# Kernel tuning notes

Hardware: AMD Instinct MI355X
Metric: run time of the kernel (lower is better)

Reference implementation:

```python
import jax, jax.numpy as jnp
import numpy as np
from functools import partial

B, T, P, W = 32, 4096, 512, 128
NMEL, FILT, PDIM, K = 80, 256, 64, 9
PAD = (K - 1) // 2  # original uses (kernel[0][0]-1)//2 for both convs
EPS = 1e-5


def setup_inputs() -> dict:
    key = jax.random.key(0)
    ks = jax.random.split(key, 8)
    inp = {}
    inp["mask"] = jnp.zeros((B, P), dtype=bool)
    inp["mels"] = jax.random.normal(ks[0], (B, T, NMEL), dtype=jnp.float32)
    inp["mel_mask"] = jnp.zeros((B, T), dtype=bool)
    # uniform segments: 8 frames per phone (sum == T), 4 phones per word (sum == P)
    inp["durations"] = jnp.full((B, P), T // P, dtype=jnp.int32)
    inp["word_phone_len"] = jnp.full((B, W), P // W, dtype=jnp.int32)
    s1 = 1.0 / np.sqrt(NMEL * K)
    s2 = 1.0 / np.sqrt(FILT * K)
    s3 = 1.0 / np.sqrt(FILT)
    inp["conv1_w"] = jax.random.normal(ks[1], (FILT, NMEL, K), dtype=jnp.float32) * s1
    inp["conv1_b"] = jnp.zeros((FILT,), dtype=jnp.float32)
    inp["ln1_g"] = jnp.ones((FILT,), dtype=jnp.float32)
    inp["ln1_b"] = jnp.zeros((FILT,), dtype=jnp.float32)
    inp["conv2_w"] = jax.random.normal(ks[2], (FILT, FILT, K), dtype=jnp.float32) * s2
    inp["conv2_b"] = jnp.zeros((FILT,), dtype=jnp.float32)
    inp["ln2_g"] = jnp.ones((FILT,), dtype=jnp.float32)
    inp["ln2_b"] = jnp.zeros((FILT,), dtype=jnp.float32)
    inp["w1"] = jax.random.normal(ks[3], (FILT, FILT), dtype=jnp.float32) * s3
    inp["b1"] = jnp.zeros((FILT,), dtype=jnp.float32)
    inp["w2"] = jax.random.normal(ks[4], (FILT, PDIM), dtype=jnp.float32) * s3
    inp["b2"] = jnp.zeros((PDIM,), dtype=jnp.float32)
    return inp


def conv1d(x, w, b):
    # x: [B, T, Cin], w: [Cout, Cin, K] -> [B, T, Cout]
    y = jax.lax.conv_general_dilated(x.transpose(0, 2, 1), w, (1,), [(PAD, PAD)])
    return y.transpose(0, 2, 1) + b


def layernorm(x, g, b):
    m = jnp.mean(x, axis=-1, keepdims=True)
    v = jnp.mean(jnp.square(x - m), axis=-1, keepdims=True)
    return (x - m) * jax.lax.rsqrt(v + EPS) * g + b


def seg_mean(feat, lens, n_seg):
    # feat: [L, D], lens: [S] -> [n_seg, D] segment means
    bounds = jnp.cumsum(lens)
    ids = jnp.searchsorted(bounds, jnp.arange(feat.shape[0]), side="right")
    s = jax.ops.segment_sum(feat, ids, num_segments=n_seg)
    cnt = jnp.maximum(lens, 1).astype(feat.dtype)
    return s / cnt[:, None]


def expand_words(word_emb, wlens, n_out):
    # word_emb: [W, D]; scatter each word embedding across its phones -> [n_out, D]
    bounds = jnp.cumsum(wlens)
    wid = jnp.searchsorted(bounds, jnp.arange(n_out), side="right")
    return word_emb[jnp.clip(wid, 0, word_emb.shape[0] - 1)]


def reference(mask, mels, mel_mask, durations, word_phone_len,
              conv1_w, conv1_b, ln1_g, ln1_b, conv2_w, conv2_b, ln2_g, ln2_b,
              w1, b1, w2, b2):
    x = conv1d(mels, conv1_w, conv1_b)
    x = layernorm(jax.nn.relu(x), ln1_g, ln1_b)
    x = conv1d(x, conv2_w, conv2_b)
    x = layernorm(jax.nn.relu(x), ln2_g, ln2_b)  # [B, T, FILT]
    # token-wise (phone) mean pool over mel frames
    x = jax.vmap(partial(seg_mean, n_seg=P))(x, durations)  # [B, P, FILT]
    # word-level mean pool over phones
    x = jax.vmap(partial(seg_mean, n_seg=W))(x, word_phone_len)  # [B, W, FILT]
    x = jax.nn.relu(x @ w1 + b1)
    x = jax.nn.relu(x @ w2 + b2)  # [B, W, PDIM]
    # expand word embeddings back to phone level
    x = jax.vmap(partial(expand_words, n_out=P))(x, word_phone_len)  # [B, P, PDIM]
    x = jnp.where(mask[..., None], 0.0, x)
    return x
```

## Files before the change

kernel.cpp:

```cpp
#include <hip/hip_runtime.h>
#include <hip/hip_fp16.h>
#include <stdint.h>

#define B_ 32
#define T_ 4096
#define P_ 512
#define W_ 128
#define NMEL 80
#define FILT 256
#define PDIM 64
#define KW 9
#define TP8 (T_ + 8)
#define MSTR 104
#define YSTR 264
#define EPS 1e-5f

typedef unsigned short u16;
typedef __attribute__((ext_vector_type(8))) short short8;
typedef __attribute__((ext_vector_type(8))) _Float16 half8;
typedef __attribute__((ext_vector_type(4))) float f32x4;
typedef __attribute__((ext_vector_type(16))) float f32x16;

typedef const __attribute__((address_space(1))) uint32_t* gptr_t;
typedef __attribute__((address_space(3))) uint32_t* lptr_t;

__device__ __forceinline__ u16 f2h(float v){ return __half_as_ushort(__float2half(v)); }

#define MFMA32(accv, av, bv) \
  accv = __builtin_amdgcn_mfma_f32_32x32x16_f16((av), (bv), (accv), 0, 0, 0)

__global__ void pack_w(const float* __restrict__ w1, const float* __restrict__ w2,
                       u16* __restrict__ Wp1, u16* __restrict__ Wp2){
  int i = blockIdx.x * 256 + threadIdx.x;
  const int N1 = KW * 12 * FILT;
  const int N2 = KW * 32 * FILT;
  if (i < N1){
    int tap = i / (12*FILT); int r = i - tap*12*FILT; int kg = r / FILT; int co = r - kg*FILT;
    short8 v;
    #pragma unroll
    for (int e=0;e<8;e++){
      int ci = kg*8 + e;
      float x = (ci < NMEL) ? w1[(co*NMEL + ci)*KW + tap] : 0.f;
      v[e] = (short)f2h(x);
    }
    *(short8*)(Wp1 + (size_t)i*8) = v;
  } else if (i < N1 + N2){
    int j = i - N1;
    int tap = j / (32*FILT); int r = j - tap*32*FILT; int kg = r / FILT; int co = r - kg*FILT;
    short8 v;
    #pragma unroll
    for (int e=0;e<8;e++){
      int ci = kg*8 + e;
      v[e] = (short)f2h(w2[(co*FILT + ci)*KW + tap]);
    }
    *(short8*)(Wp2 + (size_t)j*8) = v;
  }
}

__global__ void prep_mels(const float* __restrict__ mels, u16* __restrict__ melsPad){
  int idx = blockIdx.x * 256 + threadIdx.x;
  if (idx >= B_*TP8*13) return;
  int ch = idx % 13; int r = idx / 13; int row = r % TP8; int b = r / TP8;
  int t = row - 4;
  short8 v = (short8){0,0,0,0,0,0,0,0};
  if (t >= 0 && t < T_ && ch < 10){
    const float* src = mels + ((size_t)b*T_ + t)*NMEL + ch*8;
    const f32x4 f0 = *(const f32x4*)src;
    const f32x4 f1 = *(const f32x4*)(src+4);
    #pragma unroll
    for (int j=0;j<4;j++){ v[j]=(short)f2h(f0[j]); v[4+j]=(short)f2h(f1[j]); }
  }
  *(short8*)(melsPad + (size_t)idx*8) = v;
}

__global__ void prep_seg(const int* __restrict__ dur, const int* __restrict__ wpl,
                         int* __restrict__ wcum,
                         int* __restrict__ pid, int* __restrict__ wid,
                         u16* __restrict__ y1Pad){
  int b = blockIdx.x; int tid = threadIdx.x;
  __shared__ int dc[P_];
  __shared__ int wc[W_];
  for (int p=tid; p<P_; p+=256) dc[p] = dur[b*P_+p];
  if (tid < W_) wc[tid] = wpl[b*W_+tid];
  __syncthreads();
  if (tid == 0){ int run=0; for (int p=0;p<P_;p++){ run += dc[p]; dc[p]=run; } }
  if (tid == 64){ int run=0; for (int w=0;w<W_;w++){ run += wc[w]; wc[w]=run; wcum[b*W_+w]=run; } }
  __syncthreads();
  for (int t=tid; t<T_; t+=256){
    int lo=0, hi=P_;
    while (lo < hi){ int mid=(lo+hi)>>1; if (dc[mid] > t) hi=mid; else lo=mid+1; }
    pid[b*T_+t] = lo;
  }
  for (int p=tid; p<P_; p+=256){
    int lo=0, hi=W_;
    while (lo < hi){ int mid=(lo+hi)>>1; if (wc[mid] > p) hi=mid; else lo=mid+1; }
    wid[b*P_+p] = min(lo, W_-1);
  }
  for (int i=tid; i<8*YSTR; i+=256){
    int rr = i / YSTR; int cc = i - rr*YSTR;
    int row = (rr < 4) ? rr : (T_ + rr);
    y1Pad[((size_t)b*TP8 + row)*YSTR + cc] = 0;
  }
}

__global__ __launch_bounds__(512, 4) void conv1_k(
    const u16* __restrict__ melsPad, const u16* __restrict__ Wp1,
    const float* __restrict__ bias, const float* __restrict__ lng,
    const float* __restrict__ lnb, u16* __restrict__ y1Pad){
  __shared__ __align__(16) u16 sA[14144];
  __shared__ float sred[512], sred2[512], smean[128], srstd[128];
  const int tid = threadIdx.x;
  const int wave = tid >> 6, lane = tid & 63, l31 = lane & 31, h = lane >> 5;
  const int rg = wave >> 2, cg = wave & 3;
  const int b = blockIdx.y, t0 = blockIdx.x * 128;

  float bcol[2], gcol[2], btcol[2];
  #pragma unroll
  for (int n=0;n<2;n++){
    int c = cg*64 + n*32 + l31;
    bcol[n]=bias[c]; gcol[n]=lng[c]; btcol[n]=lnb[c];
  }

  {
    const char* gA = (const char*)(melsPad + ((size_t)b*TP8 + t0)*MSTR);
    #pragma unroll
    for (int it=0; it<4; ++it)
      if (it*8192 + tid*16 < 28288)
        __builtin_amdgcn_global_load_lds((gptr_t)(gA + it*8192 + (wave<<10) + (lane<<4)),
                                         (lptr_t)((char*)sA + it*8192 + (wave<<10)), 16, 0, 0);
  }
  const char* gB = (const char*)Wp1 + h*4096 + cg*1024 + (l31<<4);
  __syncthreads();

  f32x16 acc[2][2] = {};

  #pragma unroll 2
  for (int cc=0; cc<27; ++cc){
    const int tap = cc/3, s = cc - tap*3;
    const u16* pA = sA + ((size_t)(rg*64 + l31 + tap))*MSTR + s*32 + h*8;
    half8 a00 = *(const half8*)(pA);
    half8 a01 = *(const half8*)(pA + 16);
    half8 a10 = *(const half8*)(pA + 32*MSTR);
    half8 a11 = *(const half8*)(pA + 32*MSTR + 16);
    const char* nb = gB + (size_t)cc*16384;
    half8 b00 = *(const half8*)(nb);
    half8 b01 = *(const half8*)(nb + 512);
    half8 b10 = *(const half8*)(nb + 8192);
    half8 b11 = *(const half8*)(nb + 8704);
    MFMA32(acc[0][0], a00, b00); MFMA32(acc[0][1], a00, b01);
    MFMA32(acc[1][0], a10, b00); MFMA32(acc[1][1], a10, b01);
    MFMA32(acc[0][0], a01, b10); MFMA32(acc[0][1], a01, b11);
    MFMA32(acc[1][0], a11, b10); MFMA32(acc[1][1], a11, b11);
  }

  #pragma unroll
  for (int rb=0;rb<2;++rb)
    #pragma unroll
    for (int r=0;r<16;++r){
      float v0 = fmaxf(acc[rb][0][r] + bcol[0], 0.f);
      float v1 = fmaxf(acc[rb][1][r] + bcol[1], 0.f);
      float s = v0+v1, q = v0*v0+v1*v1;
      #pragma unroll
      for (int off=1; off<32; off<<=1){ s += __shfl_xor(s, off); q += __shfl_xor(q, off); }
      if (l31 == 0){ int row = rg*64 + rb*32 + (r&3) + 8*(r>>2) + 4*h;
        sred[row*4+cg]=s; sred2[row*4+cg]=q; }
    }
  __syncthreads();
  if (tid < 128){
    float ss=0.f, qq=0.f;
    #pragma unroll
    for (int w2=0; w2<4; w2++){ ss += sred[tid*4+w2]; qq += sred2[tid*4+w2]; }
    float mean = ss * (1.f/FILT);
    float var  = qq * (1.f/FILT) - mean*mean;
    smean[tid] = mean;
    srstd[tid] = rsqrtf(fmaxf(var, 0.f) + EPS);
  }
  __syncthreads();

  #pragma unroll
  for (int rb=0;rb<2;++rb)
    #pragma unroll
    for (int q=0;q<4;++q){
      const int rbase = rg*64 + rb*32 + q*8 + 4*h;
      float mn0=smean[rbase+0],mn1=smean[rbase+1],mn2=smean[rbase+2],mn3=smean[rbase+3];
      float rs0=srstd[rbase+0],rs1=srstd[rbase+1],rs2=srstd[rbase+2],rs3=srstd[rbase+3];
      #pragma unroll
      for (int cb=0;cb<2;++cb){
        int c = cg*64 + cb*32 + l31;
        float x0 = fmaxf(acc[rb][cb][q*4+0] + bcol[cb], 0.f);
        float x1 = fmaxf(acc[rb][cb][q*4+1] + bcol[cb], 0.f);
        float x2 = fmaxf(acc[rb][cb][q*4+2] + bcol[cb], 0.f);
        float x3 = fmaxf(acc[rb][cb][q*4+3] + bcol[cb], 0.f);
        u16* dst = y1Pad + ((size_t)b*TP8 + 4 + t0 + rbase)*YSTR + c;
        dst[0*YSTR] = f2h((x0-mn0)*rs0*gcol[cb]+btcol[cb]);
        dst[1*YSTR] = f2h((x1-mn1)*rs1*gcol[cb]+btcol[cb]);
        dst[2*YSTR] = f2h((x2-mn2)*rs2*gcol[cb]+btcol[cb]);
        dst[3*YSTR] = f2h((x3-mn3)*rs3*gcol[cb]+btcol[cb]);
      }
    }
}

__global__ __launch_bounds__(512, 4) void conv2_k(
    const u16* __restrict__ y1Pad, const u16* __restrict__ Wp2,
    const float* __restrict__ bias, const float* __restrict__ lng,
    const float* __restrict__ lnb, const int* __restrict__ pid,
    float* __restrict__ ps){
  __shared__ __align__(16) u16 sA[35904];
  __shared__ float sred[512], sred2[512], smean[128], srstd[128];
  __shared__ int pidT[128];
  const int tid = threadIdx.x;
  const int wave = tid >> 6, lane = tid & 63, l31 = lane & 31, h = lane >> 5;
  const int rg = wave >> 2, cg = wave & 3;
  const int b = blockIdx.y, t0 = blockIdx.x * 128;

  float bcol[2], gcol[2], btcol[2];
  #pragma unroll
  for (int n=0;n<2;n++){
    int c = cg*64 + n*32 + l31;
    bcol[n]=bias[c]; gcol[n]=lng[c]; btcol[n]=lnb[c];
  }
  if (tid < 128) pidT[tid] = pid[b*T_ + t0 + tid];

  {
    const char* gA = (const char*)(y1Pad + ((size_t)b*TP8 + t0)*YSTR);
    #pragma unroll
    for (int it=0; it<9; ++it)
      if (it*8192 + tid*16 < 71808)
        __builtin_amdgcn_global_load_lds((gptr_t)(gA + it*8192 + (wave<<10) + (lane<<4)),
                                         (lptr_t)((char*)sA + it*8192 + (wave<<10)), 16, 0, 0);
  }
  const char* gB = (const char*)Wp2 + h*4096 + cg*1024 + (l31<<4);
  __syncthreads();

  f32x16 acc[2][2] = {};

  #pragma unroll 2
  for (int cc=0; cc<72; ++cc){
    const int tap = cc>>3, sg = cc&7;
    const u16* pA = sA + ((size_t)(rg*64 + l31 + tap))*YSTR + sg*32 + h*8;
    half8 a00 = *(const half8*)(pA);
    half8 a01 = *(const half8*)(pA + 16);
    half8 a10 = *(const half8*)(pA + 32*YSTR);
    half8 a11 = *(const half8*)(pA + 32*YSTR + 16);
    const char* nb = gB + (size_t)cc*16384;
    half8 b00 = *(const half8*)(nb);
    half8 b01 = *(const half8*)(nb + 512);
    half8 b10 = *(const half8*)(nb + 8192);
    half8 b11 = *(const half8*)(nb + 8704);
    MFMA32(acc[0][0], a00, b00); MFMA32(acc[0][1], a00, b01);
    MFMA32(acc[1][0], a10, b00); MFMA32(acc[1][1], a10, b01);
    MFMA32(acc[0][0], a01, b10); MFMA32(acc[0][1], a01, b11);
    MFMA32(acc[1][0], a11, b10); MFMA32(acc[1][1], a11, b11);
  }

  #pragma unroll
  for (int rb=0;rb<2;++rb)
    #pragma unroll
    for (int r=0;r<16;++r){
      float v0 = fmaxf(acc[rb][0][r] + bcol[0], 0.f);
      float v1 = fmaxf(acc[rb][1][r] + bcol[1], 0.f);
      float s = v0+v1, q = v0*v0+v1*v1;
      #pragma unroll
      for (int off=1; off<32; off<<=1){ s += __shfl_xor(s, off); q += __shfl_xor(q, off); }
      if (l31 == 0){ int row = rg*64 + rb*32 + (r&3) + 8*(r>>2) + 4*h;
        sred[row*4+cg]=s; sred2[row*4+cg]=q; }
    }
  __syncthreads();
  if (tid < 128){
    float ss=0.f, qq=0.f;
    #pragma unroll
    for (int w2=0; w2<4; w2++){ ss += sred[tid*4+w2]; qq += sred2[tid*4+w2]; }
    float mean = ss * (1.f/FILT);
    float var  = qq * (1.f/FILT) - mean*mean;
    smean[tid] = mean;
    srstd[tid] = rsqrtf(fmaxf(var, 0.f) + EPS);
  }
  __syncthreads();

  #pragma unroll
  for (int rb=0;rb<2;++rb)
    #pragma unroll
    for (int q=0;q<4;++q){
      const int rbase = rg*64 + rb*32 + q*8 + 4*h;
      int p0v = pidT[rbase]; int fold = (p0v == pidT[rbase+3]);
      float mn0=smean[rbase+0],mn1=smean[rbase+1],mn2=smean[rbase+2],mn3=smean[rbase+3];
      float rs0=srstd[rbase+0],rs1=srstd[rbase+1],rs2=srstd[rbase+2],rs3=srstd[rbase+3];
      int pp = __shfl_xor(p0v, 32); int fp = __shfl_xor(fold, 32);
      #pragma unroll
      for (int cb=0;cb<2;++cb){
        int c = cg*64 + cb*32 + l31;
        float x0 = fmaxf(acc[rb][cb][q*4+0] + bcol[cb], 0.f);
        float x1 = fmaxf(acc[rb][cb][q*4+1] + bcol[cb], 0.f);
        float x2 = fmaxf(acc[rb][cb][q*4+2] + bcol[cb], 0.f);
        float x3 = fmaxf(acc[rb][cb][q*4+3] + bcol[cb], 0.f);
        float o0 = (x0-mn0)*rs0*gcol[cb]+btcol[cb];
        float o1 = (x1-mn1)*rs1*gcol[cb]+btcol[cb];
        float o2 = (x2-mn2)*rs2*gcol[cb]+btcol[cb];
        float o3 = (x3-mn3)*rs3*gcol[cb]+btcol[cb];
        float s4 = fold ? (o0+o1+o2+o3) : 0.f;
        float sp = __shfl_xor(s4, 32);
        float* basep = ps + (size_t)b*P_*FILT;
        if (fold){
          if (p0v < P_){
            if (fp && pp == p0v){ if (h == 0) atomicAdd(basep + (size_t)p0v*FILT + c, s4 + sp); }
            else atomicAdd(basep + (size_t)p0v*FILT + c, s4);
          }
        } else {
          int pj;
          pj = pidT[rbase+0]; if (pj < P_) atomicAdd(basep + (size_t)pj*FILT + c, o0);
          pj = pidT[rbase+1]; if (pj < P_) atomicAdd(basep + (size_t)pj*FILT + c, o1);
          pj = pidT[rbase+2]; if (pj < P_) atomicAdd(basep + (size_t)pj*FILT + c, o2);
          pj = pidT[rbase+3]; if (pj < P_) atomicAdd(basep + (size_t)pj*FILT + c, o3);
        }
      }
    }
}

#define WPB 8
__global__ __launch_bounds__(256) void word_k(
    const float* __restrict__ ps, const int* __restrict__ dur,
    const int* __restrict__ wcum, const int* __restrict__ wpl,
    const float* __restrict__ w1, const float* __restrict__ b1,
    const float* __restrict__ w2, const float* __restrict__ b2,
    float* __restrict__ wemb){
  int b = blockIdx.y, wg = blockIdx.x * WPB, tid = threadIdx.x;
  __shared__ float wvS[WPB][FILT];
  __shared__ float h1S[WPB][FILT];
  #pragma unroll
  for (int k=0;k<WPB;k++){
    int w = wg + k;
    int p1 = wcum[b*W_ + w]; int p0 = (w == 0) ? 0 : wcum[b*W_ + w - 1];
    if (p1 > P_) p1 = P_;
    int len = wpl[b*W_ + w];
    float a = 0.f;
    for (int p = p0; p < p1; ++p){
      int d = dur[b*P_ + p]; d = d < 1 ? 1 : d;
      a += ps[((size_t)(b*P_ + p))*FILT + tid] / (float)d;
    }
    wvS[k][tid] = a / (float)(len < 1 ? 1 : len);
  }
  __syncthreads();
  float acc[WPB];
  #pragma unroll
  for (int k=0;k<WPB;k++) acc[k] = b1[tid];
  for (int i=0;i<FILT;i++){
    float wcol = w1[i*FILT + tid];
    #pragma unroll
    for (int k=0;k<WPB;k++) acc[k] += wvS[k][i] * wcol;
  }
  #pragma unroll
  for (int k=0;k<WPB;k++) h1S[k][tid] = fmaxf(acc[k], 0.f);
  __syncthreads();
  int c = tid & 63, kq = tid >> 6;
  #pragma unroll
  for (int kk=kq; kk<WPB; kk+=4){
    float u = b2[c];
    for (int i=0;i<FILT;i++) u += h1S[kk][i] * w2[i*PDIM + c];
    wemb[((size_t)(b*W_ + wg + kk))*PDIM + c] = fmaxf(u, 0.f);
  }
}

__global__ void expand_k(const float* __restrict__ wemb, const int* __restrict__ wid,
                         const unsigned char* __restrict__ mask, float* __restrict__ out){
  int idx = blockIdx.x * 256 + threadIdx.x;
  if (idx >= B_*P_*16) return;
  int q = idx & 15; int p = (idx >> 4) & 511; int bb = idx >> 13;
  int w = wid[bb*P_ + p];
  f32x4 v = *(const f32x4*)(wemb + ((size_t)(bb*W_ + w))*PDIM + q*4);
  if (mask[bb*P_ + p]) v = (f32x4){0.f,0.f,0.f,0.f};
  *(f32x4*)(out + (size_t)idx*4) = v;
}

extern "C" void kernel_launch(void* const* d_in, const int* in_sizes, int n_in,
                              void* d_out, int out_size, void* d_ws, size_t ws_size,
                              hipStream_t stream) {
  const unsigned char* mask = (const unsigned char*)d_in[0];
  const float* mels = (const float*)d_in[1];
  const int*   dur  = (const int*)d_in[3];
  const int*   wpl  = (const int*)d_in[4];
  const float* c1w  = (const float*)d_in[5];
  const float* c1b  = (const float*)d_in[6];
  const float* l1g  = (const float*)d_in[7];
  const float* l1b  = (const float*)d_in[8];
  const float* c2w  = (const float*)d_in[9];
  const float* c2b  = (const float*)d_in[10];
  const float* l2g  = (const float*)d_in[11];
  const float* l2b  = (const float*)d_in[12];
  const float* w1   = (const float*)d_in[13];
  const float* b1   = (const float*)d_in[14];
  const float* w2   = (const float*)d_in[15];
  const float* b2   = (const float*)d_in[16];

  char* ws = (char*)d_ws;
  size_t off = 0;
  auto alloc = [&](size_t bytes){ void* p = ws + off; off += (bytes + 255) & ~(size_t)255; return p; };
  u16* melsPad = (u16*)alloc((size_t)B_*TP8*MSTR*2 + 32768);
  u16* y1Pad   = (u16*)alloc((size_t)B_*TP8*YSTR*2 + 32768);
  u16* Wp1     = (u16*)alloc((size_t)KW*12*FILT*8*2 + 32768);
  u16* Wp2     = (u16*)alloc((size_t)KW*32*FILT*8*2 + 32768);
  int* wcum    = (int*)alloc((size_t)B_*W_*4);
  int* pid     = (int*)alloc((size_t)B_*T_*4);
  int* wid     = (int*)alloc((size_t)B_*P_*4);
  float* psum  = (float*)alloc((size_t)B_*P_*FILT*4);
  float* wemb  = (float*)alloc((size_t)B_*W_*PDIM*4);

  hipMemsetAsync(psum, 0, (size_t)B_*P_*FILT*4, stream);
  pack_w<<<(KW*12*FILT + KW*32*FILT + 255)/256, 256, 0, stream>>>(c1w, c2w, Wp1, Wp2);
  prep_mels<<<(B_*TP8*13 + 255)/256, 256, 0, stream>>>(mels, melsPad);
  prep_seg<<<B_, 256, 0, stream>>>(dur, wpl, wcum, pid, wid, y1Pad);
  conv1_k<<<dim3(T_/128, B_), 512, 0, stream>>>(melsPad, Wp1, c1b, l1g, l1b, y1Pad);
  conv2_k<<<dim3(T_/128, B_), 512, 0, stream>>>(y1Pad, Wp2, c2b, l2g, l2b, pid, psum);
  word_k<<<dim3(W_/WPB, B_), 256, 0, stream>>>(psum, dur, wcum, wpl, w1, b1, w2, b2, wemb);
  expand_k<<<(B_*P_*16 + 255)/256, 256, 0, stream>>>(wemb, wid, mask, (float*)d_out);
}
```

Baseline: 352.9 us.

## Double conv time tile to 256 rows and reuse shared memory for LN reductions

Both conv kernels now process 256 time rows per block instead of 128. Each wave holds a 4x2 grid of 32x32 accumulators, so every weight fragment loaded from global memory feeds twice as many MFMAs. This halves weight traffic per output and shrinks the relative halo overhead. The LayerNorm reduction buffers now alias the input tile's shared memory after a barrier. In exchange, shared memory per block roughly doubles (about 139 KB for conv2), accumulator register use doubles, and launch bounds drop to 2 blocks, lowering occupancy and halving the grid to 512 blocks.

Measured after the change: 370.2 us. +4.9%, slower.

```diff
diff --git a/kernel.cpp b/kernel.cpp
--- a/kernel.cpp
+++ b/kernel.cpp
@@ -29,6 +29,29 @@
 #define MFMA32(accv, av, bv) \
   accv = __builtin_amdgcn_mfma_f32_32x32x16_f16((av), (bv), (accv), 0, 0, 0)
 
+#define K32_BODY(pA, STR) { \
+    half8 a0 = *(const half8*)(pA); \
+    half8 g0 = *(const half8*)((pA) + 16); \
+    half8 a1 = *(const half8*)((pA) + 32*STR); \
+    half8 g1 = *(const half8*)((pA) + 32*STR + 16); \
+    half8 a2 = *(const half8*)((pA) + 64*STR); \
+    half8 g2 = *(const half8*)((pA) + 64*STR + 16); \
+    half8 a3 = *(const half8*)((pA) + 96*STR); \
+    half8 g3 = *(const half8*)((pA) + 96*STR + 16); \
+    half8 b00 = *(const half8*)(gBp); \
+    half8 b01 = *(const half8*)(gBp + 512); \
+    half8 b10 = *(const half8*)(gBp + 8192); \
+    half8 b11 = *(const half8*)(gBp + 8704); \
+    gBp += 16384; \
+    MFMA32(acc[0][0], a0, b00); MFMA32(acc[0][1], a0, b01); \
+    MFMA32(acc[1][0], a1, b00); MFMA32(acc[1][1], a1, b01); \
+    MFMA32(acc[2][0], a2, b00); MFMA32(acc[2][1], a2, b01); \
+    MFMA32(acc[3][0], a3, b00); MFMA32(acc[3][1], a3, b01); \
+    MFMA32(acc[0][0], g0, b10); MFMA32(acc[0][1], g0, b11); \
+    MFMA32(acc[1][0], g1, b10); MFMA32(acc[1][1], g1, b11); \
+    MFMA32(acc[2][0], g2, b10); MFMA32(acc[2][1], g2, b11); \
+    MFMA32(acc[3][0], g3, b10); MFMA32(acc[3][1], g3, b11); }
+
 __global__ void pack_w(const float* __restrict__ w1, const float* __restrict__ w2,
                        u16* __restrict__ Wp1, u16* __restrict__ Wp2){
   int i = blockIdx.x * 256 + threadIdx.x;
@@ -103,16 +126,15 @@
   }
 }
 
-__global__ __launch_bounds__(512, 4) void conv1_k(
+__global__ __launch_bounds__(512, 2) void conv1_k(
     const u16* __restrict__ melsPad, const u16* __restrict__ Wp1,
     const float* __restrict__ bias, const float* __restrict__ lng,
     const float* __restrict__ lnb, u16* __restrict__ y1Pad){
-  __shared__ __align__(16) u16 sA[14144];
-  __shared__ float sred[512], sred2[512], smean[128], srstd[128];
+  __shared__ __align__(16) u16 sA[27456];
   const int tid = threadIdx.x;
   const int wave = tid >> 6, lane = tid & 63, l31 = lane & 31, h = lane >> 5;
   const int rg = wave >> 2, cg = wave & 3;
-  const int b = blockIdx.y, t0 = blockIdx.x * 128;
+  const int b = blockIdx.y, t0 = blockIdx.x * 256;
 
   float bcol[2], gcol[2], btcol[2];
   #pragma unroll
@@ -124,37 +146,35 @@
   {
     const char* gA = (const char*)(melsPad + ((size_t)b*TP8 + t0)*MSTR);
     #pragma unroll
-    for (int it=0; it<4; ++it)
-      if (it*8192 + tid*16 < 28288)
+    for (int it=0; it<7; ++it)
+      if (it*8192 + tid*16 < 54912)
         __builtin_amdgcn_global_load_lds((gptr_t)(gA + it*8192 + (wave<<10) + (lane<<4)),
                                          (lptr_t)((char*)sA + it*8192 + (wave<<10)), 16, 0, 0);
   }
-  const char* gB = (const char*)Wp1 + h*4096 + cg*1024 + (l31<<4);
-  __syncthreads();
-
-  f32x16 acc[2][2] = {};
-
-  #pragma unroll 2
-  for (int cc=0; cc<27; ++cc){
-    const int tap = cc/3, s = cc - tap*3;
-    const u16* pA = sA + ((size_t)(rg*64 + l31 + tap))*MSTR + s*32 + h*8;
-    half8 a00 = *(const half8*)(pA);
-    half8 a01 = *(const half8*)(pA + 16);
-    half8 a10 = *(const half8*)(pA + 32*MSTR);
-    half8 a11 = *(const half8*)(pA + 32*MSTR + 16);
-    const char* nb = gB + (size_t)cc*16384;
-    half8 b00 = *(const half8*)(nb);
-    half8 b01 = *(const half8*)(nb + 512);
-    half8 b10 = *(const half8*)(nb + 8192);
-    half8 b11 = *(const half8*)(nb + 8704);
-    MFMA32(acc[0][0], a00, b00); MFMA32(acc[0][1], a00, b01);
-    MFMA32(acc[1][0], a10, b00); MFMA32(acc[1][1], a10, b01);
-    MFMA32(acc[0][0], a01, b10); MFMA32(acc[0][1], a01, b11);
-    MFMA32(acc[1][0], a11, b10); MFMA32(acc[1][1], a11, b11);
-  }
-
-  #pragma unroll
-  for (int rb=0;rb<2;++rb)
+  const char* gBp = (const char*)Wp1 + h*4096 + cg*1024 + (l31<<4);
+  __syncthreads();
+
+  f32x16 acc[4][2] = {};
+  const u16* pArow = sA + ((size_t)(rg*128 + l31))*MSTR + h*8;
+
+  #pragma unroll 1
+  for (int tap=0; tap<KW; ++tap){
+    #pragma unroll
+    for (int s=0; s<3; ++s){
+      const u16* pA = pArow + s*32;
+      K32_BODY(pA, MSTR)
+    }
+    pArow += MSTR;
+  }
+
+  float* sred  = (float*)sA;
+  float* sred2 = sred + 1024;
+  float* smean = sred2 + 1024;
+  float* srstd = smean + 256;
+  __syncthreads();
+
+  #pragma unroll
+  for (int rb=0;rb<4;++rb)
     #pragma unroll
     for (int r=0;r<16;++r){
       float v0 = fmaxf(acc[rb][0][r] + bcol[0], 0.f);
@@ -162,11 +182,11 @@
       float s = v0+v1, q = v0*v0+v1*v1;
       #pragma unroll
       for (int off=1; off<32; off<<=1){ s += __shfl_xor(s, off); q += __shfl_xor(q, off); }
-      if (l31 == 0){ int row = rg*64 + rb*32 + (r&3) + 8*(r>>2) + 4*h;
+      if (l31 == 0){ int row = rg*128 + rb*32 + (r&3) + 8*(r>>2) + 4*h;
         sred[row*4+cg]=s; sred2[row*4+cg]=q; }
     }
   __syncthreads();
-  if (tid < 128){
+  if (tid < 256){
     float ss=0.f, qq=0.f;
     #pragma unroll
     for (int w2=0; w2<4; w2++){ ss += sred[tid*4+w2]; qq += sred2[tid*4+w2]; }
@@ -178,10 +198,10 @@
   __syncthreads();
 
   #pragma unroll
-  for (int rb=0;rb<2;++rb)
+  for (int rb=0;rb<4;++rb)
     #pragma unroll
     for (int q=0;q<4;++q){
-      const int rbase = rg*64 + rb*32 + q*8 + 4*h;
+      const int rbase = rg*128 + rb*32 + q*8 + 4*h;
       float mn0=smean[rbase+0],mn1=smean[rbase+1],mn2=smean[rbase+2],mn3=smean[rbase+3];
       float rs0=srstd[rbase+0],rs1=srstd[rbase+1],rs2=srstd[rbase+2],rs3=srstd[rbase+3];
       #pragma unroll
@@ -200,18 +220,17 @@
     }
 }
 
-__global__ __launch_bounds__(512, 4) void conv2_k(
+__global__ __launch_bounds__(512, 2) void conv2_k(
     const u16* __restrict__ y1Pad, const u16* __restrict__ Wp2,
     const float* __restrict__ bias, const float* __restrict__ lng,
     const float* __restrict__ lnb, const int* __restrict__ pid,
     float* __restrict__ ps){
-  __shared__ __align__(16) u16 sA[35904];
-  __shared__ float sred[512], sred2[512], smean[128], srstd[128];
-  __shared__ int pidT[128];
+  __shared__ __align__(16) u16 sA[69696];
+  __shared__ int pidT[256];
   const int tid = threadIdx.x;
   const int wave = tid >> 6, lane = tid & 63, l31 = lane & 31, h = lane >> 5;
   const int rg = wave >> 2, cg = wave & 3;
-  const int b = blockIdx.y, t0 = blockIdx.x * 128;
+  const int b = blockIdx.y, t0 = blockIdx.x * 256;
 
   float bcol[2], gcol[2], btcol[2];
   #pragma unroll
@@ -219,42 +238,40 @@
     int c = cg*64 + n*32 + l31;
     bcol[n]=bias[c]; gcol[n]=lng[c]; btcol[n]=lnb[c];
   }
-  if (tid < 128) pidT[tid] = pid[b*T_ + t0 + tid];
+  if (tid < 256) pidT[tid] = pid[b*T_ + t0 + tid];
 
   {
     const char* gA = (const char*)(y1Pad + ((size_t)b*TP8 + t0)*YSTR);
     #pragma unroll
-    for (int it=0; it<9; ++it)
-      if (it*8192 + tid*16 < 71808)
+    for (int it=0; it<18; ++it)
+      if (it*8192 + tid*16 < 139392)
         __builtin_amdgcn_global_load_lds((gptr_t)(gA + it*8192 + (wave<<10) + (lane<<4)),
                                          (lptr_t)((char*)sA + it*8192 + (wave<<10)), 16, 0, 0);
   }
-  const char* gB = (const char*)Wp2 + h*4096 + cg*1024 + (l31<<4);
-  __syncthreads();
-
-  f32x16 acc[2][2] = {};
-
-  #pragma unroll 2
-  for (int cc=0; cc<72; ++cc){
-    const int tap = cc>>3, sg = cc&7;
-    const u16* pA = sA + ((size_t)(rg*64 + l31 + tap))*YSTR + sg*32 + h*8;
-    half8 a00 = *(const half8*)(pA);
-    half8 a01 = *(const half8*)(pA + 16);
-    half8 a10 = *(const half8*)(pA + 32*YSTR);
-    half8 a11 = *(const half8*)(pA + 32*YSTR + 16);
-    const char* nb = gB + (size_t)cc*16384;
-    half8 b00 = *(const half8*)(nb);
-    half8 b01 = *(const half8*)(nb + 512);
-    half8 b10 = *(const half8*)(nb + 8192);
-    half8 b11 = *(const half8*)(nb + 8704);
-    MFMA32(acc[0][0], a00, b00); MFMA32(acc[0][1], a00, b01);
-    MFMA32(acc[1][0], a10, b00); MFMA32(acc[1][1], a10, b01);
-    MFMA32(acc[0][0], a01, b10); MFMA32(acc[0][1], a01, b11);
-    MFMA32(acc[1][0], a11, b10); MFMA32(acc[1][1], a11, b11);
-  }
-
-  #pragma unroll
-  for (int rb=0;rb<2;++rb)
+  const char* gBp = (const char*)Wp2 + h*4096 + cg*1024 + (l31<<4);
+  __syncthreads();
+
+  f32x16 acc[4][2] = {};
+  const u16* pArow = sA + ((size_t)(rg*128 + l31))*YSTR + h*8;
+
+  #pragma unroll 1
+  for (int tap=0; tap<KW; ++tap){
+    #pragma unroll 2
+    for (int sg=0; sg<8; ++sg){
+      const u16* pA = pArow + sg*32;
+      K32_BODY(pA, YSTR)
+    }
+    pArow += YSTR;
+  }
+
+  float* sred  = (float*)sA;
+  float* sred2 = sred + 1024;
+  float* smean = sred2 + 1024;
+  float* srstd = smean + 256;
+  __syncthreads();
+
+  #pragma unroll
+  for (int rb=0;rb<4;++rb)
     #pragma unroll
     for (int r=0;r<16;++r){
       float v0 = fmaxf(acc[rb][0][r] + bcol[0], 0.f);
@@ -262,11 +279,11 @@
       float s = v0+v1, q = v0*v0+v1*v1;
       #pragma unroll
       for (int off=1; off<32; off<<=1){ s += __shfl_xor(s, off); q += __shfl_xor(q, off); }
-      if (l31 == 0){ int row = rg*64 + rb*32 + (r&3) + 8*(r>>2) + 4*h;
+      if (l31 == 0){ int row = rg*128 + rb*32 + (r&3) + 8*(r>>2) + 4*h;
         sred[row*4+cg]=s; sred2[row*4+cg]=q; }
     }
   __syncthreads();
-  if (tid < 128){
+  if (tid < 256){
     float ss=0.f, qq=0.f;
     #pragma unroll
     for (int w2=0; w2<4; w2++){ ss += sred[tid*4+w2]; qq += sred2[tid*4+w2]; }
@@ -278,10 +295,10 @@
   __syncthreads();
 
   #pragma unroll
-  for (int rb=0;rb<2;++rb)
+  for (int rb=0;rb<4;++rb)
     #pragma unroll
     for (int q=0;q<4;++q){
-      const int rbase = rg*64 + rb*32 + q*8 + 4*h;
+      const int rbase = rg*128 + rb*32 + q*8 + 4*h;
       int p0v = pidT[rbase]; int fold = (p0v == pidT[rbase+3]);
       float mn0=smean[rbase+0],mn1=smean[rbase+1],mn2=smean[rbase+2],mn3=smean[rbase+3];
       float rs0=srstd[rbase+0],rs1=srstd[rbase+1],rs2=srstd[rbase+2],rs3=srstd[rbase+3];
@@ -408,8 +425,8 @@
   pack_w<<<(KW*12*FILT + KW*32*FILT + 255)/256, 256, 0, stream>>>(c1w, c2w, Wp1, Wp2);
   prep_mels<<<(B_*TP8*13 + 255)/256, 256, 0, stream>>>(mels, melsPad);
   prep_seg<<<B_, 256, 0, stream>>>(dur, wpl, wcum, pid, wid, y1Pad);
-  conv1_k<<<dim3(T_/128, B_), 512, 0, stream>>>(melsPad, Wp1, c1b, l1g, l1b, y1Pad);
-  conv2_k<<<dim3(T_/128, B_), 512, 0, stream>>>(y1Pad, Wp2, c2b, l2g, l2b, pid, psum);
+  conv1_k<<<dim3(T_/256, B_), 512, 0, stream>>>(melsPad, Wp1, c1b, l1g, l1b, y1Pad);
+  conv2_k<<<dim3(T_/256, B_), 512, 0, stream>>>(y1Pad, Wp2, c2b, l2g, l2b, pid, psum);
   word_k<<<dim3(W_/WPB, B_), 256, 0, stream>>>(psum, dur, wcum, wpl, w1, b1, w2, b2, wemb);
   expand_k<<<(B_*P_*16 + 255)/256, 256, 0, stream>>>(wemb, wid, mask, (float*)d_out);
 }
```
